# Kernel optimization log

Measured on AMD Instinct MI355X. Metric: run time of the kernel, lower is better.

Reference implementation:

```python
import jax, jax.numpy as jnp
import numpy as np

# anchor encoding indices: [x,y,z,log w,log l,log h,sin,cos,vx,vy,vz]
NUM_HEADS = 8
LN_EPS = 1e-5


def layer_norm(x, g, b):
    mu = jnp.mean(x, axis=-1, keepdims=True)
    var = jnp.var(x, axis=-1, keepdims=True)
    return (x - mu) * jax.lax.rsqrt(var + LN_EPS) * g + b


def align_anchors_to_frame(anchor, Tm):
    # anchor: (..., N, 11), Tm: (..., 4, 4)
    R = Tm[..., :3, :3]
    t = Tm[..., :3, 3]
    center = jnp.einsum('...ij,...nj->...ni', R, anchor[..., 0:3]) + t[..., None, :]
    size = anchor[..., 3:6]
    yaw = jnp.einsum('...ij,...nj->...ni', R[..., :2, :2], anchor[..., 6:8])
    vel = jnp.einsum('...ij,...nj->...ni', R, anchor[..., 8:11])
    return jnp.concatenate([center, size, yaw, vel], axis=-1)


def setup_inputs() -> dict:
    key = jax.random.key(0)
    ks = jax.random.split(key, 12)
    B, T, N, C, E, A = 2, 12, 1024, 256, 256, 11
    inp = {
        'seq_features': jax.random.normal(ks[0], (B, T, N, C), jnp.float32),
        'seq_anchors': jax.random.normal(ks[1], (B, T, N, A), jnp.float32),
        'T_ego_his2cur': jax.random.normal(ks[2], (B, T, 4, 4), jnp.float32),
        'Wf': jax.random.normal(ks[3], (E, C), jnp.float32) * (C ** -0.5),
        'bf': jnp.zeros((E,), jnp.float32),
        'Wa': jax.random.normal(ks[4], (E, A), jnp.float32) * (A ** -0.5),
        'ba': jnp.zeros((E,), jnp.float32),
        'Win': jax.random.normal(ks[5], (3 * E, E), jnp.float32) * (E ** -0.5),
        'bin_': jnp.zeros((3 * E,), jnp.float32),
        'gamma': jnp.ones((E,), jnp.float32),
        'beta': jnp.zeros((E,), jnp.float32),
    }
    return inp


def reference(seq_features, seq_anchors, T_ego_his2cur, Wf, bf, Wa, ba, Win, bin_, gamma, beta):
    B, T, N, C = seq_features.shape
    E = gamma.shape[0]
    H = NUM_HEADS
    D = E // H

    feat_cur = seq_features[:, 1:]    # (B,T-1,N,C)
    feat_prev = seq_features[:, :-1]
    anc_cur = seq_anchors[:, 1:]
    anc_prev = align_anchors_to_frame(seq_anchors[:, :-1], T_ego_his2cur[:, 1:])

    tok_cur = layer_norm(feat_cur @ Wf.T + bf + anc_cur @ Wa.T + ba, gamma, beta)
    tok_prev = layer_norm(feat_prev @ Wf.T + bf + anc_prev @ Wa.T + ba, gamma, beta)

    Wq, Wk = Win[:E], Win[E:2 * E]
    bq, bk = bin_[:E], bin_[E:2 * E]
    scale = np.float32(D) ** np.float32(-0.5)
    q = ((tok_cur @ Wq.T + bq) * scale).reshape(B, T - 1, N, H, D)
    k = (tok_prev @ Wk.T + bk).reshape(B, T - 1, N, H, D)

    scores = jnp.einsum('btnhd,btmhd->bthnm', q, k)  # (B,T-1,H,N,N)
    attn = jax.nn.softmax(scores, axis=-1).mean(axis=2)  # head-averaged weights

    eye = jnp.broadcast_to(jnp.eye(N, dtype=seq_features.dtype), (B, 1, N, N))
    return jnp.concatenate([eye, attn], axis=1)  # (B,T,N,N)
```

## Files before the change

kernel.cpp:

```cpp
#include <hip/hip_runtime.h>
#include <hip/hip_bf16.h>
#include <math.h>

#define LN_EPS 1e-5f

typedef short bf16x8 __attribute__((ext_vector_type(8)));
typedef float f32x4 __attribute__((ext_vector_type(4)));

__device__ inline short f2bf(float f) {
  union { float f; unsigned u; } v; v.f = f;
  unsigned r = v.u + 0x7FFFu + ((v.u >> 16) & 1u);
  return (short)(r >> 16);
}
__device__ inline float bf2f(unsigned short s) {
  union { unsigned u; float f; } v; v.u = ((unsigned)s) << 16;
  return v.f;
}
__device__ inline float fast_exp2(float x) {
#if __has_builtin(__builtin_amdgcn_exp2f)
  return __builtin_amdgcn_exp2f(x);
#else
  return __expf(x * 0.69314718056f);
#endif
}

__global__ __launch_bounds__(256) void convert_kernel(const float* __restrict__ Wf,
    const float* __restrict__ Win, short* __restrict__ Wfb, short* __restrict__ Wqkb)
{
  size_t i = ((size_t)blockIdx.x * 256 + threadIdx.x) * 8;
  const float* src;
  short* dst;
  if (i < 65536) { src = Wf + i; dst = Wfb + i; }
  else { src = Win + (i - 65536); dst = Wqkb + (i - 65536); }
  f32x4 x0 = *(const f32x4*)src;
  f32x4 x1 = *(const f32x4*)(src + 4);
  bf16x8 v;
  v[0] = f2bf(x0[0]); v[1] = f2bf(x0[1]); v[2] = f2bf(x0[2]); v[3] = f2bf(x0[3]);
  v[4] = f2bf(x1[0]); v[5] = f2bf(x1[1]); v[6] = f2bf(x1[2]); v[7] = f2bf(x1[3]);
  *(bf16x8*)dst = v;
}

__global__ __launch_bounds__(256) void feat_ln(const float* __restrict__ Af,
    const short* __restrict__ Wb, const float* __restrict__ bfv,
    const float* __restrict__ anchors, const float* __restrict__ Tego,
    const float* __restrict__ Wa, const float* __restrict__ ba,
    const float* __restrict__ gamma, const float* __restrict__ beta,
    short* __restrict__ tok_cur, short* __restrict__ tok_prev)
{
  const int which = blockIdx.y;
  const int row0 = blockIdx.x * 64;
  const int s24 = row0 >> 10;
  const int b = s24 / 12, t = s24 - b * 12;
  if (which == 0 && t == 0) return;
  if (which == 1 && t == 11) return;

  __shared__ short lda[64][40];
  __shared__ short ldb[256][40];
  __shared__ float ldWa[2816];
  __shared__ float aS[64][12];
  const int tid = threadIdx.x;
  const int wid = tid >> 6, lane = tid & 63;
  const int quad = lane >> 4, l15 = lane & 15;
  const int n0 = row0 & 1023;
  const int srow = tid >> 2, sseg = tid & 3;

  #pragma unroll
  for (int i = 0; i < 11; ++i) ldWa[tid + i * 256] = Wa[tid + i * 256];

  if (tid < 64) {
    const float* ap = anchors + ((size_t)s24 * 1024 + n0 + tid) * 11;
    float a[11];
    #pragma unroll
    for (int j = 0; j < 11; ++j) a[j] = ap[j];
    if (which == 1) {
      const float* Tm = Tego + ((size_t)b * 12 + t + 1) * 16;
      float r00 = Tm[0], r01 = Tm[1], r02 = Tm[2],  t0 = Tm[3];
      float r10 = Tm[4], r11 = Tm[5], r12 = Tm[6],  t1 = Tm[7];
      float r20 = Tm[8], r21 = Tm[9], r22 = Tm[10], t2 = Tm[11];
      float a0 = a[0], a1 = a[1], a2 = a[2];
      float a6 = a[6], a7 = a[7], a8 = a[8], a9 = a[9], a10 = a[10];
      a[0] = r00 * a0 + r01 * a1 + r02 * a2 + t0;
      a[1] = r10 * a0 + r11 * a1 + r12 * a2 + t1;
      a[2] = r20 * a0 + r21 * a1 + r22 * a2 + t2;
      a[6] = r00 * a6 + r01 * a7;
      a[7] = r10 * a6 + r11 * a7;
      a[8] = r00 * a8 + r01 * a9 + r02 * a10;
      a[9] = r10 * a8 + r11 * a9 + r12 * a10;
      a[10] = r20 * a8 + r21 * a9 + r22 * a10;
    }
    #pragma unroll
    for (int j = 0; j < 11; ++j) aS[tid][j] = a[j];
  }

  f32x4 z = {0.f, 0.f, 0.f, 0.f};
  f32x4 acc[16];
  #pragma unroll
  for (int j = 0; j < 16; ++j) acc[j] = z;

  const float* ap0 = Af + (size_t)(row0 + srow) * 256 + sseg * 8;
  const short* wp = Wb + (size_t)srow * 256 + sseg * 8;

  for (int kk = 0; kk < 256; kk += 32) {
    {
      f32x4 x0 = *(const f32x4*)(ap0 + kk);
      f32x4 x1 = *(const f32x4*)(ap0 + kk + 4);
      bf16x8 vv;
      vv[0] = f2bf(x0[0]); vv[1] = f2bf(x0[1]); vv[2] = f2bf(x0[2]); vv[3] = f2bf(x0[3]);
      vv[4] = f2bf(x1[0]); vv[5] = f2bf(x1[1]); vv[6] = f2bf(x1[2]); vv[7] = f2bf(x1[3]);
      *(bf16x8*)&lda[srow][sseg * 8] = vv;
    }
    #pragma unroll
    for (int p = 0; p < 4; ++p)
      *(bf16x8*)&ldb[srow + 64 * p][sseg * 8] =
          *(const bf16x8*)(wp + (size_t)p * 64 * 256 + kk);
    __syncthreads();
    bf16x8 af = *(const bf16x8*)&lda[wid * 16 + l15][quad * 8];
    #pragma unroll
    for (int j = 0; j < 16; ++j) {
      bf16x8 bq = *(const bf16x8*)&ldb[j * 16 + l15][quad * 8];
      acc[j] = __builtin_amdgcn_mfma_f32_16x16x32_bf16(af, bq, acc[j], 0, 0, 0);
    }
    __syncthreads();
  }

  float arow[4][11];
  #pragma unroll
  for (int r = 0; r < 4; ++r)
    #pragma unroll
    for (int jj = 0; jj < 11; ++jj)
      arow[r][jj] = aS[wid * 16 + quad * 4 + r][jj];

  float s1[4] = {0.f, 0.f, 0.f, 0.f};
  float s2[4] = {0.f, 0.f, 0.f, 0.f};
  #pragma unroll
  for (int j = 0; j < 16; ++j) {
    const int col = j * 16 + l15;
    const float cb = bfv[col] + ba[col];
    float wa[11];
    #pragma unroll
    for (int jj = 0; jj < 11; ++jj) wa[jj] = ldWa[col * 11 + jj];
    #pragma unroll
    for (int r = 0; r < 4; ++r) {
      float d = 0.f;
      #pragma unroll
      for (int jj = 0; jj < 11; ++jj) d += wa[jj] * arow[r][jj];
      float v = acc[j][r] + cb + d;
      acc[j][r] = v;
      s1[r] += v; s2[r] += v * v;
    }
  }
  #pragma unroll
  for (int r = 0; r < 4; ++r) {
    #pragma unroll
    for (int off = 1; off < 16; off <<= 1) {
      s1[r] += __shfl_xor(s1[r], off);
      s2[r] += __shfl_xor(s2[r], off);
    }
  }
  float mean[4], rstd[4];
  #pragma unroll
  for (int r = 0; r < 4; ++r) {
    mean[r] = s1[r] * (1.0f / 256.0f);
    float var = s2[r] * (1.0f / 256.0f) - mean[r] * mean[r];
    rstd[r] = rsqrtf(var + LN_EPS);
  }

  short* dst = which ? tok_prev : tok_cur;
  const size_t tokbase = which ? (size_t)(b * 11 + t) * 1024
                               : (size_t)(b * 11 + t - 1) * 1024;
  #pragma unroll
  for (int j = 0; j < 16; ++j) {
    const int col = j * 16 + l15;
    const float g = gamma[col], be = beta[col];
    #pragma unroll
    for (int r = 0; r < 4; ++r) {
      const int n = n0 + wid * 16 + quad * 4 + r;
      dst[(tokbase + n) * 256 + col] = f2bf((acc[j][r] - mean[r]) * rstd[r] * g + be);
    }
  }
}

__global__ __launch_bounds__(256) void gemm_qk(const short* __restrict__ tokc,
    const short* __restrict__ tokp, const short* __restrict__ Wqkb,
    const float* __restrict__ binv, short* __restrict__ qb, short* __restrict__ kb)
{
  const int sel = blockIdx.z;
  const short* Ap = sel ? tokp : tokc;
  const short* W = Wqkb + (size_t)sel * 65536;
  const float* bias = binv + sel * 256;
  const float alpha = sel ? 1.0f : 0.17677669529663687f * 1.4426950408889634f;
  short* Out = sel ? kb : qb;

  __shared__ short lda[128][40];
  __shared__ short ldb[128][40];
  const int tid = threadIdx.x;
  const int bm = blockIdx.x * 128, bn = blockIdx.y * 128;
  const int wid = tid >> 6, lane = tid & 63;
  const int quad = lane >> 4, l15 = lane & 15;
  const int wm = (wid & 1) * 64, wn = (wid >> 1) * 64;
  const int srow = tid >> 2, sseg = tid & 3;

  f32x4 z = {0.f, 0.f, 0.f, 0.f};
  f32x4 acc[4][4];
  #pragma unroll
  for (int i = 0; i < 4; ++i)
    #pragma unroll
    for (int j = 0; j < 4; ++j) acc[i][j] = z;

  const short* a0 = Ap + (size_t)(bm + srow) * 256 + sseg * 8;
  const short* a1 = Ap + (size_t)(bm + srow + 64) * 256 + sseg * 8;
  const short* b0 = W + (size_t)(bn + srow) * 256 + sseg * 8;
  const short* b1 = W + (size_t)(bn + srow + 64) * 256 + sseg * 8;

  for (int kk = 0; kk < 256; kk += 32) {
    *(bf16x8*)&lda[srow][sseg * 8]      = *(const bf16x8*)(a0 + kk);
    *(bf16x8*)&lda[srow + 64][sseg * 8] = *(const bf16x8*)(a1 + kk);
    *(bf16x8*)&ldb[srow][sseg * 8]      = *(const bf16x8*)(b0 + kk);
    *(bf16x8*)&ldb[srow + 64][sseg * 8] = *(const bf16x8*)(b1 + kk);
    __syncthreads();
    bf16x8 af[4], bq[4];
    #pragma unroll
    for (int i = 0; i < 4; ++i) {
      af[i] = *(const bf16x8*)&lda[wm + i * 16 + l15][quad * 8];
      bq[i] = *(const bf16x8*)&ldb[wn + i * 16 + l15][quad * 8];
    }
    #pragma unroll
    for (int i = 0; i < 4; ++i)
      #pragma unroll
      for (int j = 0; j < 4; ++j)
        acc[i][j] = __builtin_amdgcn_mfma_f32_16x16x32_bf16(af[i], bq[j], acc[i][j], 0, 0, 0);
    __syncthreads();
  }

  #pragma unroll
  for (int i = 0; i < 4; ++i)
    #pragma unroll
    for (int j = 0; j < 4; ++j)
      #pragma unroll
      for (int r = 0; r < 4; ++r) {
        int grow = bm + wm + i * 16 + quad * 4 + r;
        int gcol = bn + wn + j * 16 + l15;
        float v = (acc[i][j][r] + bias[gcol]) * alpha;
        int btr = grow >> 10, nn = grow & 1023, h = gcol >> 5, d = gcol & 31;
        Out[(((size_t)btr * 8 + h) * 1024 + nn) * 32 + d] = f2bf(v);
      }
}

__global__ __launch_bounds__(256) void denom_kernel(const short* __restrict__ q,
  const short* __restrict__ k, float* __restrict__ dinv)
{
  __shared__ short kst[2][4096];
  const int tid = threadIdx.x, wid = tid >> 6, lane = tid & 63;
  const int quad = lane >> 4, l15 = lane & 15;
  const int h = blockIdx.y, bt = blockIdx.z;
  const int n0 = blockIdx.x * 128 + wid * 32;
  const size_t base = ((size_t)bt * 8 + h) * 32768;
  bf16x8 qf0 = *(const bf16x8*)(q + base + (size_t)(n0 + l15) * 32 + quad * 8);
  bf16x8 qf1 = *(const bf16x8*)(q + base + (size_t)(n0 + 16 + l15) * 32 + quad * 8);
  const short* ksA = k + base + (size_t)(wid * 16) * 32 + lane * 8;
  const short* ksB = k + base + (size_t)((wid + 4) * 16) * 32 + lane * 8;
  const int wswz = ((lane & 3) ^ ((lane >> 3) & 3)) * 8;
  const int rswz = (quad ^ ((l15 >> 1) & 3)) * 8;
  short* lwA = &kst[0][wid * 512 + (lane >> 2) * 32 + wswz];
  short* lwB = &kst[0][(wid + 4) * 512 + (lane >> 2) * 32 + wswz];

  f32x4 z = {0.f, 0.f, 0.f, 0.f};
  float s0 = 0.f, s1 = 0.f;

  bf16x8 stA = *(const bf16x8*)ksA;
  bf16x8 stB = *(const bf16x8*)ksB;
  *(bf16x8*)lwA = stA;
  *(bf16x8*)lwB = stB;
  __syncthreads();

  #pragma unroll 1
  for (int rd = 0; rd < 8; ++rd) {
    const int buf = rd & 1;
    if (rd < 7) {
      stA = *(const bf16x8*)(ksA + (size_t)(rd + 1) * 128 * 32);
      stB = *(const bf16x8*)(ksB + (size_t)(rd + 1) * 128 * 32);
    }
    #pragma unroll
    for (int s = 0; s < 8; ++s) {
      bf16x8 kf = *(const bf16x8*)&kst[buf][s * 512 + l15 * 32 + rswz];
      f32x4 c0 = __builtin_amdgcn_mfma_f32_16x16x32_bf16(kf, qf0, z, 0, 0, 0);
      f32x4 c1 = __builtin_amdgcn_mfma_f32_16x16x32_bf16(kf, qf1, z, 0, 0, 0);
      s0 += fast_exp2(c0[0]) + fast_exp2(c0[1]) + fast_exp2(c0[2]) + fast_exp2(c0[3]);
      s1 += fast_exp2(c1[0]) + fast_exp2(c1[1]) + fast_exp2(c1[2]) + fast_exp2(c1[3]);
    }
    if (rd < 7) {
      *(bf16x8*)(lwA + ((buf ^ 1) << 12)) = stA;
      *(bf16x8*)(lwB + ((buf ^ 1) << 12)) = stB;
    }
    __syncthreads();
  }
  s0 += __shfl_xor(s0, 16); s0 += __shfl_xor(s0, 32);
  s1 += __shfl_xor(s1, 16); s1 += __shfl_xor(s1, 32);
  if (quad == 0) {
    float* dp = dinv + ((size_t)bt * 8 + h) * 1024 + n0;
    dp[l15] = 1.f / s0;
    dp[16 + l15] = 1.f / s1;
  }
}

__global__ __launch_bounds__(256) void prob_kernel(const short* __restrict__ q,
  const short* __restrict__ k, const float* __restrict__ dinv, float* __restrict__ out)
{
  __shared__ short kst[2][4096];
  const int tid = threadIdx.x, wid = tid >> 6, lane = tid & 63;
  const int quad = lane >> 4, l15 = lane & 15;
  const int bt = blockIdx.z;
  const int n0 = blockIdx.x * 128 + wid * 32;
  const int mbase = blockIdx.y * 128;
  const int b = bt / 11, t = bt - b * 11;

  bf16x8 qf0[8], qf1[8];
  float invd0[8], invd1[8];
  #pragma unroll
  for (int h = 0; h < 8; ++h) {
    const size_t base = ((size_t)bt * 8 + h) * 32768;
    qf0[h] = *(const bf16x8*)(q + base + (size_t)(n0 + l15) * 32 + quad * 8);
    qf1[h] = *(const bf16x8*)(q + base + (size_t)(n0 + 16 + l15) * 32 + quad * 8);
    invd0[h] = dinv[((size_t)bt * 8 + h) * 1024 + n0 + l15] * 0.125f;
    invd1[h] = dinv[((size_t)bt * 8 + h) * 1024 + n0 + 16 + l15] * 0.125f;
  }
  const short* ksA = k + (((size_t)bt * 8 + wid    ) * 1024 + mbase) * 32 + lane * 8;
  const short* ksB = k + (((size_t)bt * 8 + wid + 4) * 1024 + mbase) * 32 + lane * 8;
  const int wswz = ((lane & 3) ^ ((lane >> 3) & 3)) * 8;
  const int rswz = (quad ^ ((l15 >> 1) & 3)) * 8;
  short* lwA = &kst[0][wid * 512 + (lane >> 2) * 32 + wswz];
  short* lwB = &kst[0][(wid + 4) * 512 + (lane >> 2) * 32 + wswz];

  float* ob0 = out + ((size_t)(b * 12 + t + 1) * 1024 + n0 + l15) * 1024
                   + mbase + quad * 4;
  float* ob1 = ob0 + (size_t)16 * 1024;
  f32x4 z = {0.f, 0.f, 0.f, 0.f};

  bf16x8 stA = *(const bf16x8*)ksA;
  bf16x8 stB = *(const bf16x8*)ksB;
  *(bf16x8*)lwA = stA;
  *(bf16x8*)lwB = stB;
  __syncthreads();

  #pragma unroll 1
  for (int mt = 0; mt < 8; ++mt) {
    const int buf = mt & 1;
    if (mt < 7) {
      stA = *(const bf16x8*)(ksA + (size_t)(mt + 1) * 16 * 32);
      stB = *(const bf16x8*)(ksB + (size_t)(mt + 1) * 16 * 32);
    }
    f32x4 P0 = z, P1 = z;
    #pragma unroll
    for (int h = 0; h < 8; ++h) {
      bf16x8 kf = *(const bf16x8*)&kst[buf][h * 512 + l15 * 32 + rswz];
      f32x4 c0 = __builtin_amdgcn_mfma_f32_16x16x32_bf16(kf, qf0[h], z, 0, 0, 0);
      f32x4 c1 = __builtin_amdgcn_mfma_f32_16x16x32_bf16(kf, qf1[h], z, 0, 0, 0);
      #pragma unroll
      for (int r = 0; r < 4; ++r) {
        P0[r] += fast_exp2(c0[r]) * invd0[h];
        P1[r] += fast_exp2(c1[r]) * invd1[h];
      }
    }
    *(f32x4*)(ob0 + mt * 16) = P0;
    *(f32x4*)(ob1 + mt * 16) = P1;
    if (mt < 7) {
      *(bf16x8*)(lwA + ((buf ^ 1) << 12)) = stA;
      *(bf16x8*)(lwB + ((buf ^ 1) << 12)) = stB;
    }
    __syncthreads();
  }
}

__global__ __launch_bounds__(256) void eye_kernel(float* __restrict__ out) {
  int gid = blockIdx.x * 256 + threadIdx.x;
  int b = gid >> 18, rem = gid & 262143;
  int n = rem >> 8, m4 = rem & 255;
  f32x4 v = {0.f, 0.f, 0.f, 0.f};
  int c = n - m4 * 4;
  if (c >= 0 && c < 4) v[c] = 1.0f;
  *(f32x4*)(out + (size_t)b * 12582912 + (size_t)n * 1024 + m4 * 4) = v;
}

extern "C" void kernel_launch(void* const* d_in, const int* in_sizes, int n_in,
                              void* d_out, int out_size, void* d_ws, size_t ws_size,
                              hipStream_t stream)
{
  const float* sf   = (const float*)d_in[0];
  const float* sa   = (const float*)d_in[1];
  const float* te   = (const float*)d_in[2];
  const float* Wf   = (const float*)d_in[3];
  const float* bfv  = (const float*)d_in[4];
  const float* Wa   = (const float*)d_in[5];
  const float* ba   = (const float*)d_in[6];
  const float* Win  = (const float*)d_in[7];
  const float* binv = (const float*)d_in[8];
  const float* gam  = (const float*)d_in[9];
  const float* bet  = (const float*)d_in[10];
  float* out = (float*)d_out;

  char* w = (char*)d_ws;
  short* tok_cur  = (short*)w;  w += 11534336;
  short* tok_prev = (short*)w;  w += 11534336;
  short* qb       = (short*)w;  w += 11534336;
  short* kb       = (short*)w;  w += 11534336;
  float* dinv     = (float*)w;  w += 720896;
  short* Wfb      = (short*)w;  w += 131072;
  short* Wqkb     = (short*)w;  w += 262144;

  convert_kernel<<<dim3(96), 256, 0, stream>>>(Wf, Win, Wfb, Wqkb);
  feat_ln<<<dim3(384, 2), 256, 0, stream>>>(sf, Wfb, bfv, sa, te, Wa, ba, gam, bet,
                                            tok_cur, tok_prev);
  gemm_qk<<<dim3(176, 2, 2), 256, 0, stream>>>(tok_cur, tok_prev, Wqkb, binv, qb, kb);
  denom_kernel<<<dim3(8, 8, 22), 256, 0, stream>>>(qb, kb, dinv);
  prob_kernel<<<dim3(8, 8, 22), 256, 0, stream>>>(qb, kb, dinv, out);
  eye_kernel<<<dim3(2048), 256, 0, stream>>>(out);
}
```

Measured before the change: 257.9 us.

## Load MFMA operands directly from global memory in projection GEMMs, dropping LDS staging

Both the feature-projection+LayerNorm kernel and the Q/K projection GEMM now have each wave read its MFMA A and B fragments straight from global memory into registers. This removes the shared-memory tiles and the two barriers per k-step. The intent is to cut LDS traffic and synchronisation stalls. In exchange, global and L2 traffic rises because weight tiles (and activation rows in gemm_qk) are re-read by several waves, and no staging buffer is left to hide load latency. The anchor rows are also read from shared memory inside the epilogue loop instead of being cached in registers.

```diff
diff --git a/kernel.cpp b/kernel.cpp
--- a/kernel.cpp
+++ b/kernel.cpp
@@ -54,15 +54,12 @@
   if (which == 0 && t == 0) return;
   if (which == 1 && t == 11) return;
 
-  __shared__ short lda[64][40];
-  __shared__ short ldb[256][40];
   __shared__ float ldWa[2816];
   __shared__ float aS[64][12];
   const int tid = threadIdx.x;
   const int wid = tid >> 6, lane = tid & 63;
   const int quad = lane >> 4, l15 = lane & 15;
   const int n0 = row0 & 1023;
-  const int srow = tid >> 2, sseg = tid & 3;
 
   #pragma unroll
   for (int i = 0; i < 11; ++i) ldWa[tid + i * 256] = Wa[tid + i * 256];
@@ -97,38 +94,23 @@
   #pragma unroll
   for (int j = 0; j < 16; ++j) acc[j] = z;
 
-  const float* ap0 = Af + (size_t)(row0 + srow) * 256 + sseg * 8;
-  const short* wp = Wb + (size_t)srow * 256 + sseg * 8;
+  const float* arp = Af + (size_t)(row0 + wid * 16 + l15) * 256 + quad * 8;
+  const short* wrp = Wb + (size_t)l15 * 256 + quad * 8;
 
   for (int kk = 0; kk < 256; kk += 32) {
-    {
-      f32x4 x0 = *(const f32x4*)(ap0 + kk);
-      f32x4 x1 = *(const f32x4*)(ap0 + kk + 4);
-      bf16x8 vv;
-      vv[0] = f2bf(x0[0]); vv[1] = f2bf(x0[1]); vv[2] = f2bf(x0[2]); vv[3] = f2bf(x0[3]);
-      vv[4] = f2bf(x1[0]); vv[5] = f2bf(x1[1]); vv[6] = f2bf(x1[2]); vv[7] = f2bf(x1[3]);
-      *(bf16x8*)&lda[srow][sseg * 8] = vv;
-    }
-    #pragma unroll
-    for (int p = 0; p < 4; ++p)
-      *(bf16x8*)&ldb[srow + 64 * p][sseg * 8] =
-          *(const bf16x8*)(wp + (size_t)p * 64 * 256 + kk);
-    __syncthreads();
-    bf16x8 af = *(const bf16x8*)&lda[wid * 16 + l15][quad * 8];
+    f32x4 x0 = *(const f32x4*)(arp + kk);
+    f32x4 x1 = *(const f32x4*)(arp + kk + 4);
+    bf16x8 af;
+    af[0] = f2bf(x0[0]); af[1] = f2bf(x0[1]); af[2] = f2bf(x0[2]); af[3] = f2bf(x0[3]);
+    af[4] = f2bf(x1[0]); af[5] = f2bf(x1[1]); af[6] = f2bf(x1[2]); af[7] = f2bf(x1[3]);
     #pragma unroll
     for (int j = 0; j < 16; ++j) {
-      bf16x8 bq = *(const bf16x8*)&ldb[j * 16 + l15][quad * 8];
+      bf16x8 bq = *(const bf16x8*)(wrp + (size_t)j * 16 * 256 + kk);
       acc[j] = __builtin_amdgcn_mfma_f32_16x16x32_bf16(af, bq, acc[j], 0, 0, 0);
     }
-    __syncthreads();
-  }
-
-  float arow[4][11];
-  #pragma unroll
-  for (int r = 0; r < 4; ++r)
-    #pragma unroll
-    for (int jj = 0; jj < 11; ++jj)
-      arow[r][jj] = aS[wid * 16 + quad * 4 + r][jj];
+  }
+
+  __syncthreads();
 
   float s1[4] = {0.f, 0.f, 0.f, 0.f};
   float s2[4] = {0.f, 0.f, 0.f, 0.f};
@@ -141,9 +123,10 @@
     for (int jj = 0; jj < 11; ++jj) wa[jj] = ldWa[col * 11 + jj];
     #pragma unroll
     for (int r = 0; r < 4; ++r) {
+      const float* as = aS[wid * 16 + quad * 4 + r];
       float d = 0.f;
       #pragma unroll
-      for (int jj = 0; jj < 11; ++jj) d += wa[jj] * arow[r][jj];
+      for (int jj = 0; jj < 11; ++jj) d += wa[jj] * as[jj];
       float v = acc[j][r] + cb + d;
       acc[j][r] = v;
       s1[r] += v; s2[r] += v * v;
@@ -191,14 +174,11 @@
   const float alpha = sel ? 1.0f : 0.17677669529663687f * 1.4426950408889634f;
   short* Out = sel ? kb : qb;
 
-  __shared__ short lda[128][40];
-  __shared__ short ldb[128][40];
   const int tid = threadIdx.x;
   const int bm = blockIdx.x * 128, bn = blockIdx.y * 128;
   const int wid = tid >> 6, lane = tid & 63;
   const int quad = lane >> 4, l15 = lane & 15;
   const int wm = (wid & 1) * 64, wn = (wid >> 1) * 64;
-  const int srow = tid >> 2, sseg = tid & 3;
 
   f32x4 z = {0.f, 0.f, 0.f, 0.f};
   f32x4 acc[4][4];
@@ -207,29 +187,22 @@
     #pragma unroll
     for (int j = 0; j < 4; ++j) acc[i][j] = z;
 
-  const short* a0 = Ap + (size_t)(bm + srow) * 256 + sseg * 8;
-  const short* a1 = Ap + (size_t)(bm + srow + 64) * 256 + sseg * 8;
-  const short* b0 = W + (size_t)(bn + srow) * 256 + sseg * 8;
-  const short* b1 = W + (size_t)(bn + srow + 64) * 256 + sseg * 8;
+  const short* arp = Ap + (size_t)(bm + wm + l15) * 256 + quad * 8;
+  const short* brp = W + (size_t)(bn + wn + l15) * 256 + quad * 8;
 
   for (int kk = 0; kk < 256; kk += 32) {
-    *(bf16x8*)&lda[srow][sseg * 8]      = *(const bf16x8*)(a0 + kk);
-    *(bf16x8*)&lda[srow + 64][sseg * 8] = *(const bf16x8*)(a1 + kk);
-    *(bf16x8*)&ldb[srow][sseg * 8]      = *(const bf16x8*)(b0 + kk);
-    *(bf16x8*)&ldb[srow + 64][sseg * 8] = *(const bf16x8*)(b1 + kk);
-    __syncthreads();
     bf16x8 af[4], bq[4];
     #pragma unroll
-    for (int i = 0; i < 4; ++i) {
-      af[i] = *(const bf16x8*)&lda[wm + i * 16 + l15][quad * 8];
-      bq[i] = *(const bf16x8*)&ldb[wn + i * 16 + l15][quad * 8];
-    }
+    for (int i = 0; i < 4; ++i)
+      af[i] = *(const bf16x8*)(arp + (size_t)i * 16 * 256 + kk);
+    #pragma unroll
+    for (int j = 0; j < 4; ++j)
+      bq[j] = *(const bf16x8*)(brp + (size_t)j * 16 * 256 + kk);
     #pragma unroll
     for (int i = 0; i < 4; ++i)
       #pragma unroll
       for (int j = 0; j < 4; ++j)
         acc[i][j] = __builtin_amdgcn_mfma_f32_16x16x32_bf16(af[i], bq[j], acc[i][j], 0, 0, 0);
-    __syncthreads();
   }
 
   #pragma unroll
```

Result: slower. 302.7 us (+17.3%).

## Load A fragments directly into registers and transpose anchor-projection LDS layout

Applied to the files above, without the earlier changes.

The feat_ln kernel no longer stages the fp32 feature tile through LDS. Each lane loads its own MFMA A-fragment from global memory, converts it to bf16, and prefetches the next k-step while the weight tile is written to LDS. The anchor projection weights and anchor values are stored transposed in LDS, so the 11-term anchor dot product becomes conflict-free vector reads accumulated straight into the MFMA accumulators. Launch bounds now ask for 4 blocks per CU. These changes trade less LDS use and fewer bank conflicts for more register pressure and less coalesced global reads of the feature tile.

```diff
diff --git a/kernel.cpp b/kernel.cpp
--- a/kernel.cpp
+++ b/kernel.cpp
@@ -40,7 +40,7 @@
   *(bf16x8*)dst = v;
 }
 
-__global__ __launch_bounds__(256) void feat_ln(const float* __restrict__ Af,
+__global__ __launch_bounds__(256, 4) void feat_ln(const float* __restrict__ Af,
     const short* __restrict__ Wb, const float* __restrict__ bfv,
     const float* __restrict__ anchors, const float* __restrict__ Tego,
     const float* __restrict__ Wa, const float* __restrict__ ba,
@@ -54,19 +54,22 @@
   if (which == 0 && t == 0) return;
   if (which == 1 && t == 11) return;
 
-  __shared__ short lda[64][40];
   __shared__ short ldb[256][40];
-  __shared__ float ldWa[2816];
-  __shared__ float aS[64][12];
+  __shared__ float ldWaT[11][256];
+  __shared__ float aST[11][64];
   const int tid = threadIdx.x;
   const int wid = tid >> 6, lane = tid & 63;
   const int quad = lane >> 4, l15 = lane & 15;
   const int n0 = row0 & 1023;
   const int srow = tid >> 2, sseg = tid & 3;
 
-  #pragma unroll
-  for (int i = 0; i < 11; ++i) ldWa[tid + i * 256] = Wa[tid + i * 256];
-
+  {
+    float wv[11];
+    #pragma unroll
+    for (int jj = 0; jj < 11; ++jj) wv[jj] = Wa[(size_t)tid * 11 + jj];
+    #pragma unroll
+    for (int jj = 0; jj < 11; ++jj) ldWaT[jj][tid] = wv[jj];
+  }
   if (tid < 64) {
     const float* ap = anchors + ((size_t)s24 * 1024 + n0 + tid) * 11;
     float a[11];
@@ -89,7 +92,7 @@
       a[10] = r20 * a8 + r21 * a9 + r22 * a10;
     }
     #pragma unroll
-    for (int j = 0; j < 11; ++j) aS[tid][j] = a[j];
+    for (int j = 0; j < 11; ++j) aST[j][tid] = a[j];
   }
 
   f32x4 z = {0.f, 0.f, 0.f, 0.f};
@@ -97,24 +100,31 @@
   #pragma unroll
   for (int j = 0; j < 16; ++j) acc[j] = z;
 
-  const float* ap0 = Af + (size_t)(row0 + srow) * 256 + sseg * 8;
-  const short* wp = Wb + (size_t)srow * 256 + sseg * 8;
-
-  for (int kk = 0; kk < 256; kk += 32) {
-    {
-      f32x4 x0 = *(const f32x4*)(ap0 + kk);
-      f32x4 x1 = *(const f32x4*)(ap0 + kk + 4);
-      bf16x8 vv;
-      vv[0] = f2bf(x0[0]); vv[1] = f2bf(x0[1]); vv[2] = f2bf(x0[2]); vv[3] = f2bf(x0[3]);
-      vv[4] = f2bf(x1[0]); vv[5] = f2bf(x1[1]); vv[6] = f2bf(x1[2]); vv[7] = f2bf(x1[3]);
-      *(bf16x8*)&lda[srow][sseg * 8] = vv;
-    }
-    #pragma unroll
-    for (int p = 0; p < 4; ++p)
-      *(bf16x8*)&ldb[srow + 64 * p][sseg * 8] =
-          *(const bf16x8*)(wp + (size_t)p * 64 * 256 + kk);
-    __syncthreads();
-    bf16x8 af = *(const bf16x8*)&lda[wid * 16 + l15][quad * 8];
+  const float* arp = Af + (size_t)(row0 + wid * 16 + l15) * 256 + quad * 8;
+  const short* wgp = Wb + (size_t)srow * 256 + sseg * 8;
+
+  f32x4 xa0 = *(const f32x4*)(arp);
+  f32x4 xa1 = *(const f32x4*)(arp + 4);
+
+  #pragma unroll 1
+  for (int ks = 0; ks < 8; ++ks) {
+    const int kk = ks * 32;
+    bf16x8 w0 = *(const bf16x8*)(wgp + kk);
+    bf16x8 w1 = *(const bf16x8*)(wgp + 64 * 256 + kk);
+    bf16x8 w2 = *(const bf16x8*)(wgp + 128 * 256 + kk);
+    bf16x8 w3 = *(const bf16x8*)(wgp + 192 * 256 + kk);
+    bf16x8 af;
+    af[0] = f2bf(xa0[0]); af[1] = f2bf(xa0[1]); af[2] = f2bf(xa0[2]); af[3] = f2bf(xa0[3]);
+    af[4] = f2bf(xa1[0]); af[5] = f2bf(xa1[1]); af[6] = f2bf(xa1[2]); af[7] = f2bf(xa1[3]);
+    if (ks < 7) {
+      xa0 = *(const f32x4*)(arp + kk + 32);
+      xa1 = *(const f32x4*)(arp + kk + 36);
+    }
+    *(bf16x8*)&ldb[srow][sseg * 8]       = w0;
+    *(bf16x8*)&ldb[srow + 64][sseg * 8]  = w1;
+    *(bf16x8*)&ldb[srow + 128][sseg * 8] = w2;
+    *(bf16x8*)&ldb[srow + 192][sseg * 8] = w3;
+    __syncthreads();
     #pragma unroll
     for (int j = 0; j < 16; ++j) {
       bf16x8 bq = *(const bf16x8*)&ldb[j * 16 + l15][quad * 8];
@@ -123,12 +133,17 @@
     __syncthreads();
   }
 
-  float arow[4][11];
-  #pragma unroll
-  for (int r = 0; r < 4; ++r)
-    #pragma unroll
-    for (int jj = 0; jj < 11; ++jj)
-      arow[r][jj] = aS[wid * 16 + quad * 4 + r][jj];
+  const int rbase = wid * 16 + quad * 4;
+  #pragma unroll
+  for (int jj = 0; jj < 11; ++jj) {
+    f32x4 av = *(const f32x4*)&aST[jj][rbase];
+    #pragma unroll
+    for (int j = 0; j < 16; ++j) {
+      float wv = ldWaT[jj][j * 16 + l15];
+      #pragma unroll
+      for (int r = 0; r < 4; ++r) acc[j][r] += wv * av[r];
+    }
+  }
 
   float s1[4] = {0.f, 0.f, 0.f, 0.f};
   float s2[4] = {0.f, 0.f, 0.f, 0.f};
@@ -136,15 +151,9 @@
   for (int j = 0; j < 16; ++j) {
     const int col = j * 16 + l15;
     const float cb = bfv[col] + ba[col];
-    float wa[11];
-    #pragma unroll
-    for (int jj = 0; jj < 11; ++jj) wa[jj] = ldWa[col * 11 + jj];
     #pragma unroll
     for (int r = 0; r < 4; ++r) {
-      float d = 0.f;
-      #pragma unroll
-      for (int jj = 0; jj < 11; ++jj) d += wa[jj] * arow[r][jj];
-      float v = acc[j][r] + cb + d;
+      float v = acc[j][r] + cb;
       acc[j][r] = v;
       s1[r] += v; s2[r] += v * v;
     }
```

Result: slower. 327.9 us (+27.1%).
